# Kernel optimization log

Hardware: AMD Instinct MI355X
Metric: run time of the kernel (lower is better)

## Reference

```python
import jax, jax.numpy as jnp
import numpy as np

N = 131072
K = 27
FIN = 3
FOUT = 32
EPS = 1e-5


def _bn(h, gamma, beta, mean, var):
    return (h - mean) * jax.lax.rsqrt(var + EPS) * gamma + beta


def setup_inputs() -> dict:
    key = jax.random.key(0)
    ks = jax.random.split(key, 8)
    return {
        "x_feats": jax.random.normal(ks[0], (N, FIN), jnp.float32),
        "z_feats": jax.random.normal(ks[1], (N, FIN), jnp.float32),
        "nbr_idx": jax.random.randint(ks[2], (N, K), 0, N, jnp.int32),
        "w1": jax.random.normal(ks[3], (K, FIN, FOUT), jnp.float32) * 0.2,
        "bn1_gamma": jnp.ones((FOUT,), jnp.float32),
        "bn1_beta": jnp.zeros((FOUT,), jnp.float32),
        "bn1_mean": jax.random.normal(ks[4], (FOUT,), jnp.float32) * 0.1,
        "bn1_var": jax.random.uniform(ks[5], (FOUT,), jnp.float32, 0.5, 1.5),
        "w2": jax.random.normal(ks[6], (K, FOUT, FOUT), jnp.float32) * 0.1,
        "mlp_w": jax.random.normal(ks[7], (FIN, FOUT), jnp.float32) * 0.3,
        "mlp_b": jnp.zeros((FOUT,), jnp.float32),
        "mlp_gamma": jnp.ones((FOUT,), jnp.float32),
        "mlp_beta": jnp.zeros((FOUT,), jnp.float32),
        "mlp_mean": jnp.zeros((FOUT,), jnp.float32),
        "mlp_var": jnp.ones((FOUT,), jnp.float32),
    }


def reference(x_feats, z_feats, nbr_idx, w1, bn1_gamma, bn1_beta, bn1_mean,
              bn1_var, w2, mlp_w, mlp_b, mlp_gamma, mlp_beta, mlp_mean,
              mlp_var):
    # --- voxel branch: sparse conv (gather-GEMM) -> BN -> SiLU -> sparse conv
    g1 = x_feats[nbr_idx]                       # [N, K, FIN] irregular gather
    h = jnp.einsum('nkf,kfo->no', g1, w1)       # [N, FOUT]
    h = jax.nn.silu(_bn(h, bn1_gamma, bn1_beta, bn1_mean, bn1_var))
    g2 = h[nbr_idx]                             # [N, K, FOUT] irregular gather
    x_out = jnp.einsum('nkf,kfo->no', g2, w2)   # [N, FOUT]

    # --- point branch: SharedMLP = Linear -> BN -> ReLU
    z = z_feats @ mlp_w + mlp_b
    z = jax.nn.relu(_bn(z, mlp_gamma, mlp_beta, mlp_mean, mlp_var))

    # --- mixed_mix: fuse voxel and point features additively
    fused = x_out + z
    return (fused, fused)
```

## Files before the change

### kernel.cpp

```cpp
#include <hip/hip_runtime.h>
#include <math.h>

#define NN 131072
#define KK 27
#define FIN 3
#define FOUT 32
#define EPS 1e-5f

typedef _Float16 f16;
typedef __attribute__((ext_vector_type(8))) _Float16 f16x8;
typedef __attribute__((ext_vector_type(16))) float f32x16;

__global__ __launch_bounds__(256) void pack_w2_kernel(
    const float* __restrict__ w2, f16* __restrict__ w2p)
{
    const int t = blockIdx.x * 256 + threadIdx.x;
    if (t >= KK * 2 * 64 * 8) return;
    const int k    = t >> 10;
    const int rem  = t & 1023;
    const int half = rem >> 9;
    const int l    = (rem >> 3) & 63;
    const int j    = rem & 7;
    const int krow = half * 16 + ((l >> 5) << 3) + j;
    const int n    = l & 31;
    w2p[t] = (f16)w2[k * (FOUT * FOUT) + krow * FOUT + n];
}

__global__ __launch_bounds__(256) void conv1_kernel(
    const float* __restrict__ x_feats,
    const int*   __restrict__ nbr_idx,
    const float* __restrict__ w1,
    const float* __restrict__ g1,  const float* __restrict__ b1,
    const float* __restrict__ m1,  const float* __restrict__ v1,
    f16* __restrict__ h_out)
{
    const int n = blockIdx.x * 256 + threadIdx.x;

    int idxs[KK];
    const int* nb = nbr_idx + (size_t)n * KK;
#pragma unroll
    for (int k = 0; k < KK; ++k) idxs[k] = nb[k];

    float acc[FOUT];
#pragma unroll
    for (int o = 0; o < FOUT; ++o) acc[o] = 0.f;

#pragma unroll
    for (int c = 0; c < 3; ++c) {
        float xs[9][3];
#pragma unroll
        for (int q = 0; q < 9; ++q) {
            const float* xr = x_feats + (size_t)idxs[c * 9 + q] * FIN;
            xs[q][0] = xr[0]; xs[q][1] = xr[1]; xs[q][2] = xr[2];
        }
#pragma unroll
        for (int q = 0; q < 9; ++q) {
            const float* w = w1 + (c * 9 + q) * (FIN * FOUT);
#pragma unroll
            for (int o = 0; o < FOUT; ++o) {
                float a = acc[o];
                a = fmaf(xs[q][0], w[o],            a);
                a = fmaf(xs[q][1], w[FOUT + o],     a);
                a = fmaf(xs[q][2], w[2 * FOUT + o], a);
                acc[o] = a;
            }
        }
    }

    f16* hr = h_out + (size_t)n * FOUT;
#pragma unroll
    for (int g = 0; g < 4; ++g) {
        f16x8 hv;
#pragma unroll
        for (int j = 0; j < 8; ++j) {
            const int o = g * 8 + j;
            const float sc = g1[o] * rsqrtf(v1[o] + EPS);
            float v = (acc[o] - m1[o]) * sc + b1[o];
            v = v / (1.f + __expf(-v));
            hv[j] = (f16)v;
        }
        *(f16x8*)(hr + g * 8) = hv;
    }
}

__global__ __launch_bounds__(256) void conv2_mfma_kernel(
    const f16*   __restrict__ h,
    const int*   __restrict__ nbr_idx,
    const f16*   __restrict__ w2p,
    const float* __restrict__ z_feats,
    const float* __restrict__ mlp_w,
    const float* __restrict__ mlp_b,
    const float* __restrict__ mg, const float* __restrict__ mbe,
    const float* __restrict__ mm, const float* __restrict__ mv,
    float* __restrict__ out)
{
    const int lane = threadIdx.x & 63;
    const int wave = threadIdx.x >> 6;
    const int base = (blockIdx.x * 4 + wave) * 32;
    const int row  = lane & 31;
    const int hi   = lane >> 5;

    int idxs[KK];
    const int* nb = nbr_idx + (size_t)(base + row) * KK;
#pragma unroll
    for (int k = 0; k < KK; ++k) idxs[k] = nb[k];

    f32x16 acc0 = {};
    f32x16 acc1 = {};

    const f16x8* bp = (const f16x8*)w2p;

    const f16* hr0 = h + (size_t)idxs[0] * FOUT + hi * 8;
    f16x8 a1 = *(const f16x8*)hr0;
    f16x8 a2 = *(const f16x8*)(hr0 + 16);
    f16x8 b1 = bp[lane];
    f16x8 b2 = bp[64 + lane];

#pragma unroll
    for (int k = 0; k < KK; ++k) {
        f16x8 na1, na2, nb1, nb2;
        if (k + 1 < KK) {
            const f16* hr = h + (size_t)idxs[k + 1] * FOUT + hi * 8;
            na1 = *(const f16x8*)hr;
            na2 = *(const f16x8*)(hr + 16);
            nb1 = bp[(k + 1) * 128 + lane];
            nb2 = bp[(k + 1) * 128 + 64 + lane];
        }
        __builtin_amdgcn_s_setprio(1);
        acc0 = __builtin_amdgcn_mfma_f32_32x32x16_f16(a1, b1, acc0, 0, 0, 0);
        acc1 = __builtin_amdgcn_mfma_f32_32x32x16_f16(a2, b2, acc1, 0, 0, 0);
        __builtin_amdgcn_s_setprio(0);
        a1 = na1; a2 = na2; b1 = nb1; b2 = nb2;
    }

    const int n0 = lane & 31;
    const float wc0 = mlp_w[n0];
    const float wc1 = mlp_w[FOUT + n0];
    const float wc2 = mlp_w[2 * FOUT + n0];
    const float sc  = mg[n0] * rsqrtf(mv[n0] + EPS);
    const float bi  = mlp_b[n0];
    const float mmv = mm[n0];
    const float mbv = mbe[n0];

#pragma unroll
    for (int r = 0; r < 16; ++r) {
        const int m    = (r & 3) + ((r >> 2) << 3) + (hi << 2);
        const int node = base + m;
        const float* zr = z_feats + (size_t)node * FIN;
        float z = bi;
        z = fmaf(zr[0], wc0, z);
        z = fmaf(zr[1], wc1, z);
        z = fmaf(zr[2], wc2, z);
        z = (z - mmv) * sc + mbv;
        z = fmaxf(z, 0.f);
        const float v = acc0[r] + acc1[r] + z;
        out[(size_t)node * FOUT + n0] = v;
        out[(size_t)NN * FOUT + (size_t)node * FOUT + n0] = v;
    }
}

extern "C" void kernel_launch(void* const* d_in, const int* in_sizes, int n_in,
                              void* d_out, int out_size, void* d_ws, size_t ws_size,
                              hipStream_t stream) {
    const float* x_feats = (const float*)d_in[0];
    const float* z_feats = (const float*)d_in[1];
    const int*   nbr_idx = (const int*)d_in[2];
    const float* w1      = (const float*)d_in[3];
    const float* bn1_g   = (const float*)d_in[4];
    const float* bn1_b   = (const float*)d_in[5];
    const float* bn1_m   = (const float*)d_in[6];
    const float* bn1_v   = (const float*)d_in[7];
    const float* w2      = (const float*)d_in[8];
    const float* mlp_w   = (const float*)d_in[9];
    const float* mlp_b   = (const float*)d_in[10];
    const float* mlp_g   = (const float*)d_in[11];
    const float* mlp_be  = (const float*)d_in[12];
    const float* mlp_m   = (const float*)d_in[13];
    const float* mlp_v   = (const float*)d_in[14];

    f16* h   = (f16*)d_ws;
    f16* w2p = (f16*)((char*)d_ws + (size_t)8 * 1024 * 1024);
    float* out = (float*)d_out;

    pack_w2_kernel<<<(KK * 1024 + 255) / 256, 256, 0, stream>>>(w2, w2p);
    conv1_kernel<<<NN / 256, 256, 0, stream>>>(x_feats, nbr_idx, w1,
                                               bn1_g, bn1_b, bn1_m, bn1_v, h);
    conv2_mfma_kernel<<<NN / 128, 256, 0, stream>>>(h, nbr_idx, w2p, z_feats,
                                                    mlp_w, mlp_b, mlp_g, mlp_be,
                                                    mlp_m, mlp_v, out);
}
```

Before: 173.5 us.

## Split neighbor K-loop across thread halves and pad x to float4

Both conv kernels now split the 27 neighbor offsets into two halves of 14 and 13. Each half is handled by a different thread group (conv1) or wave (conv2), and the partial sums are reduced through shared memory. The intent is to double the number of threads in flight, which helps hide the latency of the irregular gathers. conv1 also gathers x from a float4-padded copy made by a new pad kernel, giving one vector load per neighbor instead of three scalar loads. The cost is an extra kernel launch, shared-memory reductions with a sync, and half the threads idling during the epilogue.

```diff
diff --git a/kernel.cpp b/kernel.cpp
--- a/kernel.cpp
+++ b/kernel.cpp
@@ -26,46 +26,87 @@
     w2p[t] = (f16)w2[k * (FOUT * FOUT) + krow * FOUT + n];
 }
 
+__global__ __launch_bounds__(256) void pad_x_kernel(
+    const float* __restrict__ x, float4* __restrict__ xp)
+{
+    const int n = blockIdx.x * 256 + threadIdx.x;
+    if (n >= NN) return;
+    const float* r = x + (size_t)n * 3;
+    xp[n] = make_float4(r[0], r[1], r[2], 0.f);
+}
+
+template<bool PADX>
 __global__ __launch_bounds__(256) void conv1_kernel(
-    const float* __restrict__ x_feats,
-    const int*   __restrict__ nbr_idx,
-    const float* __restrict__ w1,
+    const float*  __restrict__ x_feats,
+    const float4* __restrict__ xpad,
+    const int*    __restrict__ nbr_idx,
+    const float*  __restrict__ w1,
     const float* __restrict__ g1,  const float* __restrict__ b1,
     const float* __restrict__ m1,  const float* __restrict__ v1,
     f16* __restrict__ h_out)
 {
-    const int n = blockIdx.x * 256 + threadIdx.x;
-
-    int idxs[KK];
-    const int* nb = nbr_idx + (size_t)n * KK;
-#pragma unroll
-    for (int k = 0; k < KK; ++k) idxs[k] = nb[k];
+    __shared__ float racc[FOUT][128];
+
+    const int tid   = threadIdx.x;
+    const int khalf = tid >> 7;
+    const int ln    = tid & 127;
+    const int n     = blockIdx.x * 128 + ln;
+    const int kb    = khalf * 14;
+    const int kn    = khalf ? 13 : 14;
+
+    int idxs[14];
+    const int* nb = nbr_idx + (size_t)n * KK + kb;
+#pragma unroll
+    for (int i = 0; i < 14; ++i)
+        if (i < kn) idxs[i] = nb[i];
+    __builtin_amdgcn_sched_barrier(0);
 
     float acc[FOUT];
 #pragma unroll
     for (int o = 0; o < FOUT; ++o) acc[o] = 0.f;
 
 #pragma unroll
-    for (int c = 0; c < 3; ++c) {
-        float xs[9][3];
-#pragma unroll
-        for (int q = 0; q < 9; ++q) {
-            const float* xr = x_feats + (size_t)idxs[c * 9 + q] * FIN;
-            xs[q][0] = xr[0]; xs[q][1] = xr[1]; xs[q][2] = xr[2];
-        }
-#pragma unroll
-        for (int q = 0; q < 9; ++q) {
-            const float* w = w1 + (c * 9 + q) * (FIN * FOUT);
-#pragma unroll
-            for (int o = 0; o < FOUT; ++o) {
-                float a = acc[o];
-                a = fmaf(xs[q][0], w[o],            a);
-                a = fmaf(xs[q][1], w[FOUT + o],     a);
-                a = fmaf(xs[q][2], w[2 * FOUT + o], a);
-                acc[o] = a;
+    for (int c = 0; c < 2; ++c) {
+        float xs[7][3];
+#pragma unroll
+        for (int q = 0; q < 7; ++q) {
+            const int i = c * 7 + q;
+            if (i < kn) {
+                if (PADX) {
+                    const float4 v = xpad[idxs[i]];
+                    xs[q][0] = v.x; xs[q][1] = v.y; xs[q][2] = v.z;
+                } else {
+                    const float* xr = x_feats + (size_t)idxs[i] * FIN;
+                    xs[q][0] = xr[0]; xs[q][1] = xr[1]; xs[q][2] = xr[2];
+                }
             }
         }
-    }
+#pragma unroll
+        for (int q = 0; q < 7; ++q) {
+            const int i = c * 7 + q;
+            if (i < kn) {
+                const float* w = w1 + (kb + i) * (FIN * FOUT);
+#pragma unroll
+                for (int o = 0; o < FOUT; ++o) {
+                    float a = acc[o];
+                    a = fmaf(xs[q][0], w[o],            a);
+                    a = fmaf(xs[q][1], w[FOUT + o],     a);
+                    a = fmaf(xs[q][2], w[2 * FOUT + o], a);
+                    acc[o] = a;
+                }
+            }
+        }
+    }
+
+    if (khalf) {
+#pragma unroll
+        for (int o = 0; o < FOUT; ++o) racc[o][ln] = acc[o];
+    }
+    __syncthreads();
+    if (khalf) return;
+
+#pragma unroll
+    for (int o = 0; o < FOUT; ++o) acc[o] += racc[o][ln];
 
     f16* hr = h_out + (size_t)n * FOUT;
 #pragma unroll
@@ -94,44 +135,67 @@
     const float* __restrict__ mm, const float* __restrict__ mv,
     float* __restrict__ out)
 {
+    __shared__ float red[2][16][64];
+
     const int lane = threadIdx.x & 63;
     const int wave = threadIdx.x >> 6;
-    const int base = (blockIdx.x * 4 + wave) * 32;
+    const int pair = wave >> 1;
+    const int kodd = wave & 1;
+    const int base = (blockIdx.x * 2 + pair) * 32;
     const int row  = lane & 31;
     const int hi   = lane >> 5;
 
-    int idxs[KK];
-    const int* nb = nbr_idx + (size_t)(base + row) * KK;
-#pragma unroll
-    for (int k = 0; k < KK; ++k) idxs[k] = nb[k];
+    const int kb = kodd ? 14 : 0;
+    const int kn = kodd ? 13 : 14;
+
+    int idxs[14];
+    const int* nb = nbr_idx + (size_t)(base + row) * KK + kb;
+#pragma unroll
+    for (int i = 0; i < 14; ++i)
+        if (i < kn) idxs[i] = nb[i];
+    __builtin_amdgcn_sched_barrier(0);
 
     f32x16 acc0 = {};
     f32x16 acc1 = {};
 
-    const f16x8* bp = (const f16x8*)w2p;
-
-    const f16* hr0 = h + (size_t)idxs[0] * FOUT + hi * 8;
-    f16x8 a1 = *(const f16x8*)hr0;
-    f16x8 a2 = *(const f16x8*)(hr0 + 16);
-    f16x8 b1 = bp[lane];
-    f16x8 b2 = bp[64 + lane];
-
-#pragma unroll
-    for (int k = 0; k < KK; ++k) {
-        f16x8 na1, na2, nb1, nb2;
-        if (k + 1 < KK) {
-            const f16* hr = h + (size_t)idxs[k + 1] * FOUT + hi * 8;
+    const f16x8* bpk = (const f16x8*)w2p + (size_t)kb * 128;
+
+    f16x8 a1, a2, b1, b2;
+    {
+        const f16* hr = h + (size_t)idxs[0] * FOUT + hi * 8;
+        a1 = *(const f16x8*)hr;
+        a2 = *(const f16x8*)(hr + 16);
+        b1 = bpk[lane];
+        b2 = bpk[64 + lane];
+    }
+
+#pragma unroll
+    for (int i = 0; i < 14; ++i) {
+        if (i >= kn) break;
+        f16x8 na1, na2;
+        const bool more = (i + 1 < kn);
+        if (more) {
+            const f16* hr = h + (size_t)idxs[i + 1] * FOUT + hi * 8;
             na1 = *(const f16x8*)hr;
             na2 = *(const f16x8*)(hr + 16);
-            nb1 = bp[(k + 1) * 128 + lane];
-            nb2 = bp[(k + 1) * 128 + 64 + lane];
         }
         __builtin_amdgcn_s_setprio(1);
         acc0 = __builtin_amdgcn_mfma_f32_32x32x16_f16(a1, b1, acc0, 0, 0, 0);
         acc1 = __builtin_amdgcn_mfma_f32_32x32x16_f16(a2, b2, acc1, 0, 0, 0);
         __builtin_amdgcn_s_setprio(0);
-        a1 = na1; a2 = na2; b1 = nb1; b2 = nb2;
-    }
+        if (more) {
+            a1 = na1; a2 = na2;
+            b1 = bpk[(i + 1) * 128 + lane];
+            b2 = bpk[(i + 1) * 128 + 64 + lane];
+        }
+    }
+
+    if (!kodd) {
+#pragma unroll
+        for (int r = 0; r < 16; ++r) red[pair][r][lane] = acc0[r] + acc1[r];
+    }
+    __syncthreads();
+    if (!kodd) return;
 
     const int n0 = lane & 31;
     const float wc0 = mlp_w[n0];
@@ -153,7 +217,7 @@
         z = fmaf(zr[2], wc2, z);
         z = (z - mmv) * sc + mbv;
         z = fmaxf(z, 0.f);
-        const float v = acc0[r] + acc1[r] + z;
+        const float v = acc0[r] + acc1[r] + red[pair][r][lane] + z;
         out[(size_t)node * FOUT + n0] = v;
         out[(size_t)NN * FOUT + (size_t)node * FOUT + n0] = v;
     }
@@ -178,14 +242,26 @@
     const float* mlp_m   = (const float*)d_in[13];
     const float* mlp_v   = (const float*)d_in[14];
 
-    f16* h   = (f16*)d_ws;
-    f16* w2p = (f16*)((char*)d_ws + (size_t)8 * 1024 * 1024);
+    const size_t OFF_W2P  = (size_t)8 * 1024 * 1024;
+    const size_t OFF_XPAD = (size_t)9 * 1024 * 1024;
+    const size_t XPAD_SZ  = (size_t)NN * 16;
+
+    f16*    h    = (f16*)d_ws;
+    f16*    w2p  = (f16*)((char*)d_ws + OFF_W2P);
+    float4* xpad = (float4*)((char*)d_ws + OFF_XPAD);
+    const bool padx = ws_size >= OFF_XPAD + XPAD_SZ;
     float* out = (float*)d_out;
 
     pack_w2_kernel<<<(KK * 1024 + 255) / 256, 256, 0, stream>>>(w2, w2p);
-    conv1_kernel<<<NN / 256, 256, 0, stream>>>(x_feats, nbr_idx, w1,
-                                               bn1_g, bn1_b, bn1_m, bn1_v, h);
-    conv2_mfma_kernel<<<NN / 128, 256, 0, stream>>>(h, nbr_idx, w2p, z_feats,
-                                                    mlp_w, mlp_b, mlp_g, mlp_be,
-                                                    mlp_m, mlp_v, out);
-}
+    if (padx) {
+        pad_x_kernel<<<NN / 256, 256, 0, stream>>>(x_feats, xpad);
+        conv1_kernel<true><<<NN / 128, 256, 0, stream>>>(
+            x_feats, xpad, nbr_idx, w1, bn1_g, bn1_b, bn1_m, bn1_v, h);
+    } else {
+        conv1_kernel<false><<<NN / 128, 256, 0, stream>>>(
+            x_feats, xpad, nbr_idx, w1, bn1_g, bn1_b, bn1_m, bn1_v, h);
+    }
+    conv2_mfma_kernel<<<NN / 64, 256, 0, stream>>>(h, nbr_idx, w2p, z_feats,
+                                                   mlp_w, mlp_b, mlp_g, mlp_be,
+                                                   mlp_m, mlp_v, out);
+}
```

Measured after the change: 312.1 us. 79.9% more time.

## Split conv1 neighbor loop across two thread halves, pad x to float4, deepen conv2 prefetch

Applied to the files above, without the earlier changes.

conv1 now assigns two threads per node, each handling half of the 27 neighbors (padded to 28 with zero weights), and reduces the partial sums through shared memory. x_feats is padded into float4 rows so each neighbor gather is a single 16-byte load. conv2 prefetches neighbor rows six steps ahead instead of one, and asm barriers pin the index loads. The aim is more parallelism and memory-level concurrency on the irregular gathers. The cost is an extra padding kernel, shared-memory traffic and higher register pressure.

```diff
diff --git a/kernel.cpp b/kernel.cpp
--- a/kernel.cpp
+++ b/kernel.cpp
@@ -3,6 +3,7 @@
 
 #define NN 131072
 #define KK 27
+#define KP 28
 #define FIN 3
 #define FOUT 32
 #define EPS 1e-5f
@@ -11,61 +12,98 @@
 typedef __attribute__((ext_vector_type(8))) _Float16 f16x8;
 typedef __attribute__((ext_vector_type(16))) float f32x16;
 
-__global__ __launch_bounds__(256) void pack_w2_kernel(
-    const float* __restrict__ w2, f16* __restrict__ w2p)
+__global__ __launch_bounds__(256) void pack_kernel(
+    const float* __restrict__ w2, const float* __restrict__ w1,
+    f16* __restrict__ w2p, float* __restrict__ w1p)
 {
     const int t = blockIdx.x * 256 + threadIdx.x;
-    if (t >= KK * 2 * 64 * 8) return;
-    const int k    = t >> 10;
-    const int rem  = t & 1023;
-    const int half = rem >> 9;
-    const int l    = (rem >> 3) & 63;
-    const int j    = rem & 7;
-    const int krow = half * 16 + ((l >> 5) << 3) + j;
-    const int n    = l & 31;
-    w2p[t] = (f16)w2[k * (FOUT * FOUT) + krow * FOUT + n];
+    if (t < KP * 1024) {
+        const int k    = t >> 10;
+        const int rem  = t & 1023;
+        const int half = rem >> 9;
+        const int l    = (rem >> 3) & 63;
+        const int j    = rem & 7;
+        const int krow = half * 16 + ((l >> 5) << 3) + j;
+        const int n    = l & 31;
+        w2p[t] = (k < KK) ? (f16)w2[k * (FOUT * FOUT) + krow * FOUT + n]
+                          : (f16)0.f;
+    } else {
+        const int u = t - KP * 1024;
+        if (u < KP * FIN * FOUT) {
+            const int k = u / (FIN * FOUT);
+            w1p[u] = (k < KK) ? w1[u] : 0.f;
+        }
+    }
+}
+
+__global__ __launch_bounds__(256) void pad_x_kernel(
+    const float* __restrict__ x, float4* __restrict__ xp)
+{
+    const int n = blockIdx.x * 256 + threadIdx.x;
+    if (n >= NN) return;
+    const float* r = x + (size_t)n * 3;
+    xp[n] = make_float4(r[0], r[1], r[2], 0.f);
 }
 
 __global__ __launch_bounds__(256) void conv1_kernel(
-    const float* __restrict__ x_feats,
-    const int*   __restrict__ nbr_idx,
-    const float* __restrict__ w1,
+    const float4* __restrict__ xpad,
+    const int*    __restrict__ nbr_idx,
+    const float*  __restrict__ w1p,
     const float* __restrict__ g1,  const float* __restrict__ b1,
     const float* __restrict__ m1,  const float* __restrict__ v1,
     f16* __restrict__ h_out)
 {
-    const int n = blockIdx.x * 256 + threadIdx.x;
-
-    int idxs[KK];
-    const int* nb = nbr_idx + (size_t)n * KK;
-#pragma unroll
-    for (int k = 0; k < KK; ++k) idxs[k] = nb[k];
+    __shared__ float racc[FOUT][128];
+
+    const int tid   = threadIdx.x;
+    const int khalf = tid >> 7;
+    const int ln    = tid & 127;
+    const int n     = blockIdx.x * 128 + ln;
+    const int kb    = khalf * 14;
+
+    int idxs[14];
+    const int* nb = nbr_idx + (size_t)n * KK + kb;
+#pragma unroll
+    for (int i = 0; i < 14; ++i) {
+        const int off = (kb + i < KK) ? i : 0;
+        idxs[i] = nb[off];
+    }
+#pragma unroll
+    for (int i = 0; i < 14; ++i) asm volatile("" : "+v"(idxs[i]));
 
     float acc[FOUT];
 #pragma unroll
     for (int o = 0; o < FOUT; ++o) acc[o] = 0.f;
 
 #pragma unroll
-    for (int c = 0; c < 3; ++c) {
-        float xs[9][3];
-#pragma unroll
-        for (int q = 0; q < 9; ++q) {
-            const float* xr = x_feats + (size_t)idxs[c * 9 + q] * FIN;
-            xs[q][0] = xr[0]; xs[q][1] = xr[1]; xs[q][2] = xr[2];
-        }
-#pragma unroll
-        for (int q = 0; q < 9; ++q) {
-            const float* w = w1 + (c * 9 + q) * (FIN * FOUT);
+    for (int c = 0; c < 2; ++c) {
+        float4 xs[7];
+#pragma unroll
+        for (int q = 0; q < 7; ++q)
+            xs[q] = xpad[idxs[c * 7 + q]];
+#pragma unroll
+        for (int q = 0; q < 7; ++q) {
+            const float* w = w1p + (kb + c * 7 + q) * (FIN * FOUT);
 #pragma unroll
             for (int o = 0; o < FOUT; ++o) {
                 float a = acc[o];
-                a = fmaf(xs[q][0], w[o],            a);
-                a = fmaf(xs[q][1], w[FOUT + o],     a);
-                a = fmaf(xs[q][2], w[2 * FOUT + o], a);
+                a = fmaf(xs[q].x, w[o],            a);
+                a = fmaf(xs[q].y, w[FOUT + o],     a);
+                a = fmaf(xs[q].z, w[2 * FOUT + o], a);
                 acc[o] = a;
             }
         }
     }
+
+    if (khalf) {
+#pragma unroll
+        for (int o = 0; o < FOUT; ++o) racc[o][ln] = acc[o];
+    }
+    __syncthreads();
+    if (khalf) return;
+
+#pragma unroll
+    for (int o = 0; o < FOUT; ++o) acc[o] += racc[o][ln];
 
     f16* hr = h_out + (size_t)n * FOUT;
 #pragma unroll
@@ -104,33 +142,37 @@
     const int* nb = nbr_idx + (size_t)(base + row) * KK;
 #pragma unroll
     for (int k = 0; k < KK; ++k) idxs[k] = nb[k];
+#pragma unroll
+    for (int k = 0; k < KK; ++k) asm volatile("" : "+v"(idxs[k]));
 
     f32x16 acc0 = {};
     f32x16 acc1 = {};
 
     const f16x8* bp = (const f16x8*)w2p;
 
-    const f16* hr0 = h + (size_t)idxs[0] * FOUT + hi * 8;
-    f16x8 a1 = *(const f16x8*)hr0;
-    f16x8 a2 = *(const f16x8*)(hr0 + 16);
-    f16x8 b1 = bp[lane];
-    f16x8 b2 = bp[64 + lane];
+    constexpr int D = 6;
+    f16x8 A1[KK], A2[KK];
+
+#pragma unroll
+    for (int k = 0; k < D; ++k) {
+        const f16* hr = h + (size_t)idxs[k] * FOUT + hi * 8;
+        A1[k] = *(const f16x8*)hr;
+        A2[k] = *(const f16x8*)(hr + 16);
+    }
 
 #pragma unroll
     for (int k = 0; k < KK; ++k) {
-        f16x8 na1, na2, nb1, nb2;
-        if (k + 1 < KK) {
-            const f16* hr = h + (size_t)idxs[k + 1] * FOUT + hi * 8;
-            na1 = *(const f16x8*)hr;
-            na2 = *(const f16x8*)(hr + 16);
-            nb1 = bp[(k + 1) * 128 + lane];
-            nb2 = bp[(k + 1) * 128 + 64 + lane];
-        }
+        if (k + D < KK) {
+            const f16* hr = h + (size_t)idxs[k + D] * FOUT + hi * 8;
+            A1[k + D] = *(const f16x8*)hr;
+            A2[k + D] = *(const f16x8*)(hr + 16);
+        }
+        const f16x8 b1 = bp[k * 128 + lane];
+        const f16x8 b2 = bp[k * 128 + 64 + lane];
         __builtin_amdgcn_s_setprio(1);
-        acc0 = __builtin_amdgcn_mfma_f32_32x32x16_f16(a1, b1, acc0, 0, 0, 0);
-        acc1 = __builtin_amdgcn_mfma_f32_32x32x16_f16(a2, b2, acc1, 0, 0, 0);
+        acc0 = __builtin_amdgcn_mfma_f32_32x32x16_f16(A1[k], b1, acc0, 0, 0, 0);
+        acc1 = __builtin_amdgcn_mfma_f32_32x32x16_f16(A2[k], b2, acc1, 0, 0, 0);
         __builtin_amdgcn_s_setprio(0);
-        a1 = na1; a2 = na2; b1 = nb1; b2 = nb2;
     }
 
     const int n0 = lane & 31;
@@ -178,12 +220,20 @@
     const float* mlp_m   = (const float*)d_in[13];
     const float* mlp_v   = (const float*)d_in[14];
 
-    f16* h   = (f16*)d_ws;
-    f16* w2p = (f16*)((char*)d_ws + (size_t)8 * 1024 * 1024);
+    const size_t OFF_W2P  = (size_t)8 * 1024 * 1024;
+    const size_t OFF_W1P  = OFF_W2P + 64 * 1024;
+    const size_t OFF_XPAD = (size_t)9 * 1024 * 1024;
+
+    f16*    h    = (f16*)d_ws;
+    f16*    w2p  = (f16*)((char*)d_ws + OFF_W2P);
+    float*  w1p  = (float*)((char*)d_ws + OFF_W1P);
+    float4* xpad = (float4*)((char*)d_ws + OFF_XPAD);
     float* out = (float*)d_out;
 
-    pack_w2_kernel<<<(KK * 1024 + 255) / 256, 256, 0, stream>>>(w2, w2p);
-    conv1_kernel<<<NN / 256, 256, 0, stream>>>(x_feats, nbr_idx, w1,
+    const int pack_elems = KP * 1024 + KP * FIN * FOUT;
+    pack_kernel<<<(pack_elems + 255) / 256, 256, 0, stream>>>(w2, w1, w2p, w1p);
+    pad_x_kernel<<<NN / 256, 256, 0, stream>>>(x_feats, xpad);
+    conv1_kernel<<<NN / 128, 256, 0, stream>>>(xpad, nbr_idx, w1p,
                                                bn1_g, bn1_b, bn1_m, bn1_v, h);
     conv2_mfma_kernel<<<NN / 128, 256, 0, stream>>>(h, nbr_idx, w2p, z_feats,
                                                     mlp_w, mlp_b, mlp_g, mlp_be,
```

Measured after the change: 201.9 us. 1.16x slower.

## Fuse pack, conv1 and conv2 into persistent kernel with grid barriers

Applied to the files above, without the earlier changes.

Replaces the three separate launches with a single persistent kernel sized to occupancy, which packs w2, runs conv1, then conv2, separated by atomic-counter grid barriers. conv1 now splits the 27 neighbor taps across two thread halves and reduces them through shared memory, giving 128 nodes per block with more parallelism per node. The conv2 neighbor loop is split into two halves so fewer index registers are live at once. The aim is to cut launch gaps and register pressure. The cost is a spin-wait barrier that relies on every block being co-resident, plus an extra memset.

```diff
diff --git a/kernel.cpp b/kernel.cpp
--- a/kernel.cpp
+++ b/kernel.cpp
@@ -11,134 +11,173 @@
 typedef __attribute__((ext_vector_type(8))) _Float16 f16x8;
 typedef __attribute__((ext_vector_type(16))) float f32x16;
 
-__global__ __launch_bounds__(256) void pack_w2_kernel(
-    const float* __restrict__ w2, f16* __restrict__ w2p)
-{
-    const int t = blockIdx.x * 256 + threadIdx.x;
-    if (t >= KK * 2 * 64 * 8) return;
-    const int k    = t >> 10;
-    const int rem  = t & 1023;
-    const int half = rem >> 9;
-    const int l    = (rem >> 3) & 63;
-    const int j    = rem & 7;
-    const int krow = half * 16 + ((l >> 5) << 3) + j;
-    const int n    = l & 31;
-    w2p[t] = (f16)w2[k * (FOUT * FOUT) + krow * FOUT + n];
-}
-
-__global__ __launch_bounds__(256) void conv1_kernel(
-    const float* __restrict__ x_feats,
-    const int*   __restrict__ nbr_idx,
+
+__device__ __forceinline__ void pack_w2_block(
+    const float* __restrict__ w2, f16* __restrict__ w2p, int k, int t)
+{
+#pragma unroll
+    for (int r = 0; r < 4; ++r) {
+        const int e    = r * 256 + t;
+        const int half = e >> 9;
+        const int l    = (e >> 3) & 63;
+        const int j    = e & 7;
+        const int krow = half * 16 + ((l >> 5) << 3) + j;
+        const int n    = l & 31;
+        w2p[k * 1024 + e] = (f16)w2[k * (FOUT * FOUT) + krow * FOUT + n];
+    }
+}
+
+template<int KB, int KN>
+__device__ __forceinline__ void c1_accum(
+    int n, const float* __restrict__ x, const int* __restrict__ nbr,
+    const float* __restrict__ w1, float* acc)
+{
+    int idxs[KN];
+    const int* nb = nbr + (size_t)n * KK + KB;
+#pragma unroll
+    for (int i = 0; i < KN; ++i) idxs[i] = nb[i];
+#pragma unroll
+    for (int i = 0; i < KN; ++i) asm volatile("" : "+v"(idxs[i]));
+
+    constexpr int C0 = 7, C1 = KN - 7;
+    float xs[7][3];
+#pragma unroll
+    for (int q = 0; q < C0; ++q) {
+        const float* xr = x + (size_t)idxs[q] * FIN;
+        xs[q][0] = xr[0]; xs[q][1] = xr[1]; xs[q][2] = xr[2];
+    }
+#pragma unroll
+    for (int q = 0; q < C0; ++q) {
+        const float* w = w1 + (KB + q) * (FIN * FOUT);
+#pragma unroll
+        for (int o = 0; o < FOUT; ++o)
+            acc[o] = fmaf(xs[q][0], w[o],
+                     fmaf(xs[q][1], w[FOUT + o],
+                     fmaf(xs[q][2], w[2 * FOUT + o], acc[o])));
+    }
+#pragma unroll
+    for (int q = 0; q < C1; ++q) {
+        const float* xr = x + (size_t)idxs[C0 + q] * FIN;
+        xs[q][0] = xr[0]; xs[q][1] = xr[1]; xs[q][2] = xr[2];
+    }
+#pragma unroll
+    for (int q = 0; q < C1; ++q) {
+        const float* w = w1 + (KB + C0 + q) * (FIN * FOUT);
+#pragma unroll
+        for (int o = 0; o < FOUT; ++o)
+            acc[o] = fmaf(xs[q][0], w[o],
+                     fmaf(xs[q][1], w[FOUT + o],
+                     fmaf(xs[q][2], w[2 * FOUT + o], acc[o])));
+    }
+}
+
+__device__ __forceinline__ void conv1_chunk(
+    int chunk, int t,
+    const float* __restrict__ x, const int* __restrict__ nbr,
     const float* __restrict__ w1,
-    const float* __restrict__ g1,  const float* __restrict__ b1,
-    const float* __restrict__ m1,  const float* __restrict__ v1,
-    f16* __restrict__ h_out)
-{
-    const int n = blockIdx.x * 256 + threadIdx.x;
-
-    int idxs[KK];
-    const int* nb = nbr_idx + (size_t)n * KK;
-#pragma unroll
-    for (int k = 0; k < KK; ++k) idxs[k] = nb[k];
+    const float* __restrict__ g1, const float* __restrict__ b1,
+    const float* __restrict__ m1, const float* __restrict__ v1,
+    f16* __restrict__ h, float (*racc)[128])
+{
+    const int khalf = t >> 7;
+    const int ln    = t & 127;
+    const int n     = chunk * 128 + ln;
 
     float acc[FOUT];
 #pragma unroll
     for (int o = 0; o < FOUT; ++o) acc[o] = 0.f;
 
-#pragma unroll
-    for (int c = 0; c < 3; ++c) {
-        float xs[9][3];
-#pragma unroll
-        for (int q = 0; q < 9; ++q) {
-            const float* xr = x_feats + (size_t)idxs[c * 9 + q] * FIN;
-            xs[q][0] = xr[0]; xs[q][1] = xr[1]; xs[q][2] = xr[2];
+    if (khalf == 0) c1_accum<0, 14>(n, x, nbr, w1, acc);
+    else            c1_accum<14, 13>(n, x, nbr, w1, acc);
+
+    if (khalf) {
+#pragma unroll
+        for (int o = 0; o < FOUT; ++o) racc[o][ln] = acc[o];
+    }
+    __syncthreads();
+    if (!khalf) {
+#pragma unroll
+        for (int o = 0; o < FOUT; ++o) acc[o] += racc[o][ln];
+        f16* hr = h + (size_t)n * FOUT;
+#pragma unroll
+        for (int g = 0; g < 4; ++g) {
+            f16x8 hv;
+#pragma unroll
+            for (int j = 0; j < 8; ++j) {
+                const int o = g * 8 + j;
+                const float sc = g1[o] * rsqrtf(v1[o] + EPS);
+                float v = (acc[o] - m1[o]) * sc + b1[o];
+                v = v / (1.f + __expf(-v));
+                hv[j] = (f16)v;
+            }
+            *(f16x8*)(hr + g * 8) = hv;
         }
-#pragma unroll
-        for (int q = 0; q < 9; ++q) {
-            const float* w = w1 + (c * 9 + q) * (FIN * FOUT);
-#pragma unroll
-            for (int o = 0; o < FOUT; ++o) {
-                float a = acc[o];
-                a = fmaf(xs[q][0], w[o],            a);
-                a = fmaf(xs[q][1], w[FOUT + o],     a);
-                a = fmaf(xs[q][2], w[2 * FOUT + o], a);
-                acc[o] = a;
-            }
-        }
-    }
-
-    f16* hr = h_out + (size_t)n * FOUT;
-#pragma unroll
-    for (int g = 0; g < 4; ++g) {
-        f16x8 hv;
-#pragma unroll
-        for (int j = 0; j < 8; ++j) {
-            const int o = g * 8 + j;
-            const float sc = g1[o] * rsqrtf(v1[o] + EPS);
-            float v = (acc[o] - m1[o]) * sc + b1[o];
-            v = v / (1.f + __expf(-v));
-            hv[j] = (f16)v;
-        }
-        *(f16x8*)(hr + g * 8) = hv;
-    }
-}
-
-__global__ __launch_bounds__(256) void conv2_mfma_kernel(
-    const f16*   __restrict__ h,
-    const int*   __restrict__ nbr_idx,
-    const f16*   __restrict__ w2p,
-    const float* __restrict__ z_feats,
-    const float* __restrict__ mlp_w,
-    const float* __restrict__ mlp_b,
-    const float* __restrict__ mg, const float* __restrict__ mbe,
-    const float* __restrict__ mm, const float* __restrict__ mv,
-    float* __restrict__ out)
-{
-    const int lane = threadIdx.x & 63;
-    const int wave = threadIdx.x >> 6;
-    const int base = (blockIdx.x * 4 + wave) * 32;
-    const int row  = lane & 31;
-    const int hi   = lane >> 5;
-
-    int idxs[KK];
-    const int* nb = nbr_idx + (size_t)(base + row) * KK;
-#pragma unroll
-    for (int k = 0; k < KK; ++k) idxs[k] = nb[k];
-
-    f32x16 acc0 = {};
-    f32x16 acc1 = {};
-
-    const f16x8* bp = (const f16x8*)w2p;
+    }
+    __syncthreads();
+}
+
+template<int KB, int KN>
+__device__ __forceinline__ void c2_half(
+    int nrow, int hi, int lane, const f16* __restrict__ h,
+    const int* __restrict__ nbr, const f16x8* __restrict__ bp,
+    f32x16& acc0, f32x16& acc1)
+{
+    int idxs[KN];
+    const int* nb = nbr + (size_t)nrow * KK + KB;
+#pragma unroll
+    for (int i = 0; i < KN; ++i) idxs[i] = nb[i];
+#pragma unroll
+    for (int i = 0; i < KN; ++i) asm volatile("" : "+v"(idxs[i]));
 
     const f16* hr0 = h + (size_t)idxs[0] * FOUT + hi * 8;
     f16x8 a1 = *(const f16x8*)hr0;
     f16x8 a2 = *(const f16x8*)(hr0 + 16);
-    f16x8 b1 = bp[lane];
-    f16x8 b2 = bp[64 + lane];
-
-#pragma unroll
-    for (int k = 0; k < KK; ++k) {
+    f16x8 b1 = bp[KB * 128 + lane];
+    f16x8 b2 = bp[KB * 128 + 64 + lane];
+
+#pragma unroll
+    for (int i = 0; i < KN; ++i) {
         f16x8 na1, na2, nb1, nb2;
-        if (k + 1 < KK) {
-            const f16* hr = h + (size_t)idxs[k + 1] * FOUT + hi * 8;
+        if (i + 1 < KN) {
+            const f16* hr = h + (size_t)idxs[i + 1] * FOUT + hi * 8;
             na1 = *(const f16x8*)hr;
             na2 = *(const f16x8*)(hr + 16);
-            nb1 = bp[(k + 1) * 128 + lane];
-            nb2 = bp[(k + 1) * 128 + 64 + lane];
+            nb1 = bp[(KB + i + 1) * 128 + lane];
+            nb2 = bp[(KB + i + 1) * 128 + 64 + lane];
         }
         __builtin_amdgcn_s_setprio(1);
         acc0 = __builtin_amdgcn_mfma_f32_32x32x16_f16(a1, b1, acc0, 0, 0, 0);
         acc1 = __builtin_amdgcn_mfma_f32_32x32x16_f16(a2, b2, acc1, 0, 0, 0);
         __builtin_amdgcn_s_setprio(0);
-        a1 = na1; a2 = na2; b1 = nb1; b2 = nb2;
-    }
+        if (i + 1 < KN) { a1 = na1; a2 = na2; b1 = nb1; b2 = nb2; }
+    }
+}
+
+__device__ __forceinline__ void conv2_chunk(
+    int chunk, int t, const f16* __restrict__ h, const int* __restrict__ nbr,
+    const f16* __restrict__ w2p, const float* __restrict__ z,
+    const float* __restrict__ mw, const float* __restrict__ mb2,
+    const float* __restrict__ mg, const float* __restrict__ mbe,
+    const float* __restrict__ mm, const float* __restrict__ mv,
+    float* __restrict__ out)
+{
+    const int lane = t & 63;
+    const int wave = t >> 6;
+    const int base = chunk * 128 + wave * 32;
+    const int row  = lane & 31;
+    const int hi   = lane >> 5;
+
+    f32x16 acc0 = {}, acc1 = {};
+    const f16x8* bp = (const f16x8*)w2p;
+    c2_half<0, 14>(base + row, hi, lane, h, nbr, bp, acc0, acc1);
+    c2_half<14, 13>(base + row, hi, lane, h, nbr, bp, acc0, acc1);
 
     const int n0 = lane & 31;
-    const float wc0 = mlp_w[n0];
-    const float wc1 = mlp_w[FOUT + n0];
-    const float wc2 = mlp_w[2 * FOUT + n0];
+    const float wc0 = mw[n0];
+    const float wc1 = mw[FOUT + n0];
+    const float wc2 = mw[2 * FOUT + n0];
     const float sc  = mg[n0] * rsqrtf(mv[n0] + EPS);
-    const float bi  = mlp_b[n0];
+    const float bi  = mb2[n0];
     const float mmv = mm[n0];
     const float mbv = mbe[n0];
 
@@ -146,17 +185,90 @@
     for (int r = 0; r < 16; ++r) {
         const int m    = (r & 3) + ((r >> 2) << 3) + (hi << 2);
         const int node = base + m;
-        const float* zr = z_feats + (size_t)node * FIN;
-        float z = bi;
-        z = fmaf(zr[0], wc0, z);
-        z = fmaf(zr[1], wc1, z);
-        z = fmaf(zr[2], wc2, z);
-        z = (z - mmv) * sc + mbv;
-        z = fmaxf(z, 0.f);
-        const float v = acc0[r] + acc1[r] + z;
+        const float* zr = z + (size_t)node * FIN;
+        float zv = bi;
+        zv = fmaf(zr[0], wc0, zv);
+        zv = fmaf(zr[1], wc1, zv);
+        zv = fmaf(zr[2], wc2, zv);
+        zv = (zv - mmv) * sc + mbv;
+        zv = fmaxf(zv, 0.f);
+        const float v = acc0[r] + acc1[r] + zv;
         out[(size_t)node * FOUT + n0] = v;
         out[(size_t)NN * FOUT + (size_t)node * FOUT + n0] = v;
     }
+}
+
+__device__ __forceinline__ void grid_bar(unsigned* bar, unsigned target)
+{
+    __threadfence();
+    __syncthreads();
+    if (threadIdx.x == 0) {
+        __hip_atomic_fetch_add(bar, 1u, __ATOMIC_RELEASE,
+                               __HIP_MEMORY_SCOPE_AGENT);
+        while (__hip_atomic_load(bar, __ATOMIC_ACQUIRE,
+                                 __HIP_MEMORY_SCOPE_AGENT) < target)
+            __builtin_amdgcn_s_sleep(2);
+    }
+    __syncthreads();
+    __threadfence();
+}
+
+__global__ __launch_bounds__(256, 4) void fused_kernel(
+    const float* __restrict__ x, const float* __restrict__ z,
+    const int* __restrict__ nbr, const float* __restrict__ w1,
+    const float* __restrict__ g1, const float* __restrict__ b1,
+    const float* __restrict__ m1, const float* __restrict__ v1,
+    const float* __restrict__ w2,
+    const float* __restrict__ mw, const float* __restrict__ mb2,
+    const float* __restrict__ mg, const float* __restrict__ mbe,
+    const float* __restrict__ mm, const float* __restrict__ mv,
+    f16* __restrict__ h, f16* __restrict__ w2p, unsigned* __restrict__ bar,
+    float* __restrict__ out)
+{
+    __shared__ float racc[FOUT][128];
+    const int t   = threadIdx.x;
+    const int bid = blockIdx.x;
+    const int G   = gridDim.x;
+    const int NC  = NN / 128;
+
+    for (int k = bid; k < KK; k += G) pack_w2_block(w2, w2p, k, t);
+    grid_bar(bar, (unsigned)G);
+
+    for (int c = bid; c < NC; c += G)
+        conv1_chunk(c, t, x, nbr, w1, g1, b1, m1, v1, h, racc);
+    grid_bar(bar, (unsigned)(2 * G));
+
+    for (int c = bid; c < NC; c += G)
+        conv2_chunk(c, t, h, nbr, w2p, z, mw, mb2, mg, mbe, mm, mv, out);
+}
+
+__global__ __launch_bounds__(256) void pack_kernel(
+    const float* __restrict__ w2, f16* __restrict__ w2p)
+{
+    if (blockIdx.x < KK) pack_w2_block(w2, w2p, blockIdx.x, threadIdx.x);
+}
+
+__global__ __launch_bounds__(256) void conv1_kernel(
+    const float* __restrict__ x, const int* __restrict__ nbr,
+    const float* __restrict__ w1,
+    const float* __restrict__ g1, const float* __restrict__ b1,
+    const float* __restrict__ m1, const float* __restrict__ v1,
+    f16* __restrict__ h)
+{
+    __shared__ float racc[FOUT][128];
+    conv1_chunk(blockIdx.x, threadIdx.x, x, nbr, w1, g1, b1, m1, v1, h, racc);
+}
+
+__global__ __launch_bounds__(256) void conv2_kernel(
+    const f16* __restrict__ h, const int* __restrict__ nbr,
+    const f16* __restrict__ w2p, const float* __restrict__ z,
+    const float* __restrict__ mw, const float* __restrict__ mb2,
+    const float* __restrict__ mg, const float* __restrict__ mbe,
+    const float* __restrict__ mm, const float* __restrict__ mv,
+    float* __restrict__ out)
+{
+    conv2_chunk(blockIdx.x, threadIdx.x, h, nbr, w2p, z,
+                mw, mb2, mg, mbe, mm, mv, out);
 }
 
 extern "C" void kernel_launch(void* const* d_in, const int* in_sizes, int n_in,
@@ -178,14 +290,34 @@
     const float* mlp_m   = (const float*)d_in[13];
     const float* mlp_v   = (const float*)d_in[14];
 
-    f16* h   = (f16*)d_ws;
-    f16* w2p = (f16*)((char*)d_ws + (size_t)8 * 1024 * 1024);
-    float* out = (float*)d_out;
-
-    pack_w2_kernel<<<(KK * 1024 + 255) / 256, 256, 0, stream>>>(w2, w2p);
-    conv1_kernel<<<NN / 256, 256, 0, stream>>>(x_feats, nbr_idx, w1,
-                                               bn1_g, bn1_b, bn1_m, bn1_v, h);
-    conv2_mfma_kernel<<<NN / 128, 256, 0, stream>>>(h, nbr_idx, w2p, z_feats,
-                                                    mlp_w, mlp_b, mlp_g, mlp_be,
-                                                    mlp_m, mlp_v, out);
-}
+    const size_t OFF_W2P = (size_t)8 * 1024 * 1024;
+    const size_t OFF_BAR = (size_t)9 * 1024 * 1024;
+
+    f16*      h    = (f16*)d_ws;
+    f16*      w2p  = (f16*)((char*)d_ws + OFF_W2P);
+    unsigned* bar  = (unsigned*)((char*)d_ws + OFF_BAR);
+    float*    out  = (float*)d_out;
+
+    int maxB = 0;
+    hipError_t oe = hipOccupancyMaxActiveBlocksPerMultiprocessor(
+        &maxB, fused_kernel, 256, 0);
+    int G = 0;
+    if (oe == hipSuccess && maxB > 0) {
+        G = maxB * 256;
+        if (G > NN / 128) G = NN / 128;
+    }
+
+    if (G >= 256 && ws_size >= OFF_BAR + 64) {
+        hipMemsetAsync(bar, 0, sizeof(unsigned), stream);
+        fused_kernel<<<G, 256, 0, stream>>>(
+            x_feats, z_feats, nbr_idx, w1, bn1_g, bn1_b, bn1_m, bn1_v, w2,
+            mlp_w, mlp_b, mlp_g, mlp_be, mlp_m, mlp_v, h, w2p, bar, out);
+    } else {
+        pack_kernel<<<KK, 256, 0, stream>>>(w2, w2p);
+        conv1_kernel<<<NN / 128, 256, 0, stream>>>(
+            x_feats, nbr_idx, w1, bn1_g, bn1_b, bn1_m, bn1_v, h);
+        conv2_kernel<<<NN / 128, 256, 0, stream>>>(
+            h, nbr_idx, w2p, z_feats, mlp_w, mlp_b, mlp_g, mlp_be,
+            mlp_m, mlp_v, out);
+    }
+}
```

Result: slower. 427.1 us (+146.2%).
